# Kernel tuning notes

Hardware: AMD Instinct MI355X
Metric: run time of the kernel (lower is better)

Reference implementation:

```python
import jax, jax.numpy as jnp
import numpy as np

B, SQ, HID, NH, PAST = 8, 16, 1024, 16, 4096
DH = HID // NH
ROPE_BASE = 10000.0


def _rope(x, pos):
    # rotate-half RoPE applied over the full hidden dim (as in the module, rope
    # is built with hidden_size and applied before the head split)
    half = x.shape[-1] // 2
    inv_freq = 1.0 / (ROPE_BASE ** (jnp.arange(half, dtype=jnp.float32) / half))
    ang = pos[..., None].astype(jnp.float32) * inv_freq  # [B, S, half]
    cos, sin = jnp.cos(ang), jnp.sin(ang)
    x1, x2 = x[..., :half], x[..., half:]
    return jnp.concatenate([x1 * cos - x2 * sin, x2 * cos + x1 * sin], axis=-1).astype(x.dtype)


def setup_inputs() -> dict:
    key = jax.random.key(0)
    ks = jax.random.split(key, 16)
    s = 1.0 / np.sqrt(HID)
    return {
        "hidden_state": jax.random.normal(ks[0], (B, SQ, HID), jnp.float32),
        "attention_mask": jnp.zeros((B, SQ, SQ), jnp.float32),
        "past_key": jax.random.normal(ks[1], (B, NH, PAST, DH), jnp.float32),
        "past_value": jax.random.normal(ks[2], (B, NH, PAST, DH), jnp.float32),
        "position_ids": jax.random.randint(ks[3], (B, SQ), 0, 4200, jnp.int32),
        "Wq": jax.random.normal(ks[4], (HID, HID), jnp.float32) * s,
        "bq": jnp.zeros((HID,), jnp.float32),
        "Wk": jax.random.normal(ks[5], (HID, HID), jnp.float32) * s,
        "bk": jnp.zeros((HID,), jnp.float32),
        "Wv": jax.random.normal(ks[6], (HID, HID), jnp.float32) * s,
        "bv": jnp.zeros((HID,), jnp.float32),
        "Wo": jax.random.normal(ks[7], (HID, HID), jnp.float32) * s,
        "bo": jnp.zeros((HID,), jnp.float32),
    }


def reference(hidden_state, attention_mask, past_key, past_value, position_ids,
              Wq, bq, Wk, bk, Wv, bv, Wo, bo):
    b, sq, hid = hidden_state.shape
    nh = NH
    dh = hid // nh

    q = hidden_state @ Wq + bq
    k = hidden_state @ Wk + bk
    v = hidden_state @ Wv + bv

    q = _rope(q, position_ids)
    k = _rope(k, position_ids)

    # split heads -> [B, H, S, Dh]
    q = q.reshape(b, sq, nh, dh).transpose(0, 2, 1, 3)
    k = k.reshape(b, sq, nh, dh).transpose(0, 2, 1, 3)
    v = v.reshape(b, sq, nh, dh).transpose(0, 2, 1, 3)

    # KV-cache concat along the key/seq dim
    new_key = jnp.concatenate((past_key, k), axis=2)      # [B, H, Skv, Dh]
    new_value = jnp.concatenate((past_value, v), axis=2)
    skv_past = past_key.shape[2]
    mask = jnp.concatenate(
        (jnp.zeros((b, sq, skv_past), attention_mask.dtype), attention_mask), axis=2)

    scale = 1.0 / jnp.sqrt(jnp.asarray(dh, q.dtype))
    scores = jnp.einsum("bhqd,bhkd->bhqk", q, new_key) * scale + mask[:, None]
    probs = jax.nn.softmax(scores, axis=-1)
    ctx = jnp.einsum("bhqk,bhkd->bhqd", probs, new_value)  # [B, H, Sq, Dh]

    out = ctx.transpose(0, 2, 1, 3).reshape(b, sq, hid) @ Wo + bo
    return (out, new_key, new_value)
```

## Files before the change

kernel.cpp:

```cpp
#include <hip/hip_runtime.h>
#include <math.h>

#define BB   8
#define SQ   16
#define HIDD 1024
#define NHD  16
#define PAST 4096
#define DH   64
#define SKV  (PAST + SQ)
#define NTOK (BB * SQ)

__global__ __launch_bounds__(256) void gemm3(
    const float* __restrict__ A,
    const float* __restrict__ W0, const float* __restrict__ W1, const float* __restrict__ W2,
    const float* __restrict__ b0, const float* __restrict__ b1, const float* __restrict__ b2,
    float* __restrict__ O0, float* __restrict__ O1, float* __restrict__ O2)
{
    const int nt   = blockIdx.x;
    const int mt   = blockIdx.y;
    const int wsel = nt >> 4;
    const int col0 = (nt & 15) * 64;
    const int m0   = mt * 32;
    const float* W    = (wsel == 0) ? W0 : (wsel == 1) ? W1 : W2;
    const float* bias = (wsel == 0) ? b0 : (wsel == 1) ? b1 : b2;
    float*       Out  = (wsel == 0) ? O0 : (wsel == 1) ? O1 : O2;

    __shared__ float As[32][33];
    __shared__ float Bs[32][64];

    const int t    = threadIdx.x;
    const int tm   = t >> 4;
    const int tn   = t & 15;
    const int arow = t >> 3;
    const int acol = (t & 7) << 2;
    const int brow = t >> 4;
    const int bcol = (t & 15) << 2;

    float acc0[4] = {0.f,0.f,0.f,0.f};
    float acc1[4] = {0.f,0.f,0.f,0.f};

    for (int k0 = 0; k0 < HIDD; k0 += 32) {
        __syncthreads();
        float4 a4 = *(const float4*)(A + (size_t)(m0 + arow) * HIDD + k0 + acol);
        As[arow][acol+0] = a4.x; As[arow][acol+1] = a4.y;
        As[arow][acol+2] = a4.z; As[arow][acol+3] = a4.w;
        *(float4*)(&Bs[brow][bcol]) =
            *(const float4*)(W + (size_t)(k0 + brow) * HIDD + col0 + bcol);
        *(float4*)(&Bs[brow + 16][bcol]) =
            *(const float4*)(W + (size_t)(k0 + brow + 16) * HIDD + col0 + bcol);
        __syncthreads();
        #pragma unroll
        for (int kk = 0; kk < 32; ++kk) {
            const float  a0 = As[2*tm][kk];
            const float  a1 = As[2*tm + 1][kk];
            const float4 b4 = *(const float4*)(&Bs[kk][tn << 2]);
            acc0[0] += a0*b4.x; acc0[1] += a0*b4.y; acc0[2] += a0*b4.z; acc0[3] += a0*b4.w;
            acc1[0] += a1*b4.x; acc1[1] += a1*b4.y; acc1[2] += a1*b4.z; acc1[3] += a1*b4.w;
        }
    }
    const float4 bb = *(const float4*)(bias + col0 + (tn << 2));
    float* o0 = Out + (size_t)(m0 + 2*tm) * HIDD + col0 + (tn << 2);
    float* o1 = o0 + HIDD;
    o0[0] = acc0[0] + bb.x; o0[1] = acc0[1] + bb.y; o0[2] = acc0[2] + bb.z; o0[3] = acc0[3] + bb.w;
    o1[0] = acc1[0] + bb.x; o1[1] = acc1[1] + bb.y; o1[2] = acc1[2] + bb.z; o1[3] = acc1[3] + bb.w;
}

__global__ __launch_bounds__(256) void rope_scatter(
    const float* __restrict__ qr, const float* __restrict__ kr, const float* __restrict__ vr,
    const int* __restrict__ pos_ids,
    float* __restrict__ Qh, float* __restrict__ nk, float* __restrict__ nv)
{
    const int tok = blockIdx.x;
    const int b   = tok >> 4;
    const int s   = tok & 15;
    const float pos = (float)pos_ids[tok];
    const size_t rq = (size_t)tok * HIDD;
    for (int i = threadIdx.x; i < 512; i += 256) {
        const float inv = expf((float)i * (-9.210340371976184f / 512.0f));
        const float ang = pos * inv;
        const float c  = cosf(ang);
        const float sn = sinf(ang);
        const int h1 = i >> 6, d = i & 63;
        const int h2 = h1 + 8;
        float x1, x2;
        x1 = qr[rq + i]; x2 = qr[rq + i + 512];
        Qh[((size_t)(b*NHD + h1)*SQ + s)*DH + d] = x1*c - x2*sn;
        Qh[((size_t)(b*NHD + h2)*SQ + s)*DH + d] = x2*c + x1*sn;
        x1 = kr[rq + i]; x2 = kr[rq + i + 512];
        nk[((size_t)(b*NHD + h1)*SKV + PAST + s)*DH + d] = x1*c - x2*sn;
        nk[((size_t)(b*NHD + h2)*SKV + PAST + s)*DH + d] = x2*c + x1*sn;
        x1 = vr[rq + i]; x2 = vr[rq + i + 512];
        nv[((size_t)(b*NHD + h1)*SKV + PAST + s)*DH + d] = x1;
        nv[((size_t)(b*NHD + h2)*SKV + PAST + s)*DH + d] = x2;
    }
}

__global__ __launch_bounds__(256) void attn_partial(
    const float* __restrict__ pk, const float* __restrict__ pv,
    const float* __restrict__ Qh, const float* __restrict__ amask,
    float* __restrict__ nk, float* __restrict__ nv,
    float* __restrict__ pc, float* __restrict__ pm, float* __restrict__ pl)
{
    const int chunk = blockIdx.x;
    const int bh    = blockIdx.y;
    const int b     = bh >> 4;
    const int t     = threadIdx.x;
    const int w     = t >> 6;
    const int lane  = t & 63;
    const int qq    = lane >> 4;
    const int d4    = lane & 15;

    __shared__ float  Qs[SQ * DH];
    __shared__ float4 Ks[64 * 16];
    __shared__ float  Vs[64 * DH];
    __shared__ float4 Ps[4 * 64];

    {
        const int q = t >> 4, i = t & 15;
        float4 q4 = *(const float4*)(Qh + ((size_t)bh * SQ + q) * DH + 4*i);
        q4.x *= 0.125f; q4.y *= 0.125f; q4.z *= 0.125f; q4.w *= 0.125f;
        *(float4*)(&Qs[q * DH + 4*i]) = q4;
    }

    float m_r[4], l_r[4];
    #pragma unroll
    for (int q = 0; q < 4; ++q) { m_r[q] = -3.0e38f; l_r[q] = 0.0f; }
    float4 ctx = make_float4(0.f, 0.f, 0.f, 0.f);

    const int ntiles = (chunk == 7) ? 9 : 8;
    for (int tile = 0; tile < ntiles; ++tile) {
        __syncthreads();
        if (tile < 8) {
            const int k0 = chunk * 512 + tile * 64;
            #pragma unroll
            for (int p = 0; p < 4; ++p) {
                const int c = t + 256 * p;
                const int j = c >> 4, i = c & 15;
                const size_t po = ((size_t)bh * PAST + k0 + j) * DH + 4*i;
                const size_t no = ((size_t)bh * SKV  + k0 + j) * DH + 4*i;
                const float4 k4 = *(const float4*)(pk + po);
                *(float4*)(nk + no) = k4;
                Ks[j * 16 + (i ^ (j & 7))] = k4;
                const float4 v4 = *(const float4*)(pv + po);
                *(float4*)(nv + no) = v4;
                *(float4*)(&Vs[j * DH + 4*i]) = v4;
            }
        } else {
            const int j = t >> 4, i = t & 15;
            const size_t no = ((size_t)bh * SKV + PAST + j) * DH + 4*i;
            Ks[j * 16 + (i ^ (j & 7))] = *(const float4*)(nk + no);
            *(float4*)(&Vs[j * DH + 4*i]) = *(const float4*)(nv + no);
        }
        __syncthreads();

        const int jcount = (tile < 8) ? 64 : 16;

        float s[4];
        {
            float4 acc[4];
            #pragma unroll
            for (int q = 0; q < 4; ++q) acc[q] = make_float4(0.f,0.f,0.f,0.f);
            if (lane < jcount) {
                #pragma unroll
                for (int i = 0; i < 16; ++i) {
                    const float4 k4 = Ks[lane * 16 + (i ^ (lane & 7))];
                    #pragma unroll
                    for (int q = 0; q < 4; ++q) {
                        const float4 q4 = *(const float4*)(&Qs[(4*w + q) * DH + 4*i]);
                        acc[q].x += k4.x * q4.x; acc[q].y += k4.y * q4.y;
                        acc[q].z += k4.z * q4.z; acc[q].w += k4.w * q4.w;
                    }
                }
            }
            #pragma unroll
            for (int q = 0; q < 4; ++q)
                s[q] = (lane < jcount) ? (acc[q].x + acc[q].y + acc[q].z + acc[q].w)
                                       : -3.0e38f;
        }
        if (tile == 8 && lane < 16) {
            #pragma unroll
            for (int q = 0; q < 4; ++q)
                s[q] += amask[((size_t)b * SQ + 4*w + q) * SQ + lane];
        }

        float alpha[4], pjv[4];
        #pragma unroll
        for (int q = 0; q < 4; ++q) {
            float mx = s[q];
            #pragma unroll
            for (int off = 1; off < 64; off <<= 1)
                mx = fmaxf(mx, __shfl_xor(mx, off, 64));
            const float mnew = fmaxf(m_r[q], mx);
            alpha[q] = __expf(m_r[q] - mnew);
            const float p = __expf(s[q] - mnew);
            pjv[q] = p;
            float ps = p;
            #pragma unroll
            for (int off = 1; off < 64; off <<= 1)
                ps += __shfl_xor(ps, off, 64);
            l_r[q] = l_r[q] * alpha[q] + ps;
            m_r[q] = mnew;
        }
        {
            float4 pw;
            pw.x = pjv[0]; pw.y = pjv[1]; pw.z = pjv[2]; pw.w = pjv[3];
            Ps[w * 64 + lane] = pw;
        }

        const float asel = (qq == 0) ? alpha[0] : (qq == 1) ? alpha[1]
                         : (qq == 2) ? alpha[2] : alpha[3];
        ctx.x *= asel; ctx.y *= asel; ctx.z *= asel; ctx.w *= asel;

        const float* Pf = (const float*)&Ps[w * 64];
        for (int j = 0; j < jcount; ++j) {
            const float  p  = Pf[4*j + qq];
            const float4 v4 = *(const float4*)(&Vs[j * DH + 4*d4]);
            ctx.x += p * v4.x; ctx.y += p * v4.y; ctx.z += p * v4.z; ctx.w += p * v4.w;
        }
    }

    const int blk = bh * 8 + chunk;
    const int qg  = 4*w + qq;
    *(float4*)(pc + (size_t)blk * 1024 + qg * DH + 4*d4) = ctx;
    if (d4 == 0) {
        const float msel = (qq == 0) ? m_r[0] : (qq == 1) ? m_r[1] : (qq == 2) ? m_r[2] : m_r[3];
        const float lsel = (qq == 0) ? l_r[0] : (qq == 1) ? l_r[1] : (qq == 2) ? l_r[2] : l_r[3];
        pm[blk * 16 + qg] = msel;
        pl[blk * 16 + qg] = lsel;
    }
}

__global__ __launch_bounds__(256) void attn_reduce(
    const float* __restrict__ pc, const float* __restrict__ pm,
    const float* __restrict__ pl, float* __restrict__ ctxw)
{
    const int bh = blockIdx.x;
    const int b  = bh >> 4, h = bh & 15;
    const int t  = threadIdx.x;
    __shared__ float mg[SQ], li[SQ];
    if (t < SQ) {
        float m = -3.0e38f;
        #pragma unroll
        for (int c = 0; c < 8; ++c) m = fmaxf(m, pm[(bh*8 + c) * 16 + t]);
        float L = 0.f;
        #pragma unroll
        for (int c = 0; c < 8; ++c)
            L += pl[(bh*8 + c) * 16 + t] * __expf(pm[(bh*8 + c) * 16 + t] - m);
        mg[t] = m; li[t] = 1.0f / L;
    }
    __syncthreads();
    #pragma unroll
    for (int r = 0; r < 4; ++r) {
        const int idx = t + 256 * r;
        const int q = idx >> 6, d = idx & 63;
        float acc = 0.f;
        #pragma unroll
        for (int c = 0; c < 8; ++c)
            acc += pc[(size_t)(bh*8 + c) * 1024 + idx]
                 * __expf(pm[(bh*8 + c) * 16 + q] - mg[q]);
        ctxw[((size_t)(b*SQ + q) * NHD + h) * DH + d] = acc * li[q];
    }
}

extern "C" void kernel_launch(void* const* d_in, const int* in_sizes, int n_in,
                              void* d_out, int out_size, void* d_ws, size_t ws_size,
                              hipStream_t stream)
{
    const float* hidden = (const float*)d_in[0];
    const float* amask  = (const float*)d_in[1];
    const float* past_k = (const float*)d_in[2];
    const float* past_v = (const float*)d_in[3];
    const int*   pos    = (const int*)  d_in[4];
    const float* Wq = (const float*)d_in[5];  const float* bq = (const float*)d_in[6];
    const float* Wk = (const float*)d_in[7];  const float* bk = (const float*)d_in[8];
    const float* Wv = (const float*)d_in[9];  const float* bv = (const float*)d_in[10];
    const float* Wo = (const float*)d_in[11]; const float* bo = (const float*)d_in[12];

    float* out = (float*)d_out;
    float* nk  = out + (size_t)NTOK * HIDD;
    float* nv  = nk + (size_t)BB * NHD * SKV * DH;

    float* ws     = (float*)d_ws;
    float* q_raw  = ws;
    float* k_raw  = q_raw + 131072;
    float* v_raw  = k_raw + 131072;
    float* Qh     = v_raw + 131072;
    float* pc     = Qh    + 131072;
    float* pm     = pc    + 1024 * 1024;
    float* pl     = pm    + 1024 * 16;
    float* ctxw   = pl    + 1024 * 16;

    gemm3<<<dim3(48, 4), 256, 0, stream>>>(hidden, Wq, Wk, Wv, bq, bk, bv,
                                           q_raw, k_raw, v_raw);
    rope_scatter<<<NTOK, 256, 0, stream>>>(q_raw, k_raw, v_raw, pos, Qh, nk, nv);
    attn_partial<<<dim3(8, 128), 256, 0, stream>>>(past_k, past_v, Qh, amask,
                                                   nk, nv, pc, pm, pl);
    attn_reduce<<<128, 256, 0, stream>>>(pc, pm, pl, ctxw);
    gemm3<<<dim3(16, 4), 256, 0, stream>>>(ctxw, Wo, Wo, Wo, bo, bo, bo,
                                           out, out, out);
}
```

Before: 581.9 us.

## Split attention KV into more chunks and read V directly from global

```diff
diff --git a/kernel.cpp b/kernel.cpp
--- a/kernel.cpp
+++ b/kernel.cpp
@@ -76,10 +76,10 @@
     const float pos = (float)pos_ids[tok];
     const size_t rq = (size_t)tok * HIDD;
     for (int i = threadIdx.x; i < 512; i += 256) {
-        const float inv = expf((float)i * (-9.210340371976184f / 512.0f));
+        const float inv = __expf((float)i * (-9.210340371976184f / 512.0f));
         const float ang = pos * inv;
-        const float c  = cosf(ang);
-        const float sn = sinf(ang);
+        float c, sn;
+        __sincosf(ang, &sn, &c);
         const int h1 = i >> 6, d = i & 63;
         const int h2 = h1 + 8;
         float x1, x2;
@@ -95,11 +95,12 @@
     }
 }
 
-__global__ __launch_bounds__(256) void attn_partial(
+__global__ __launch_bounds__(256, 6) void attn_partial(
     const float* __restrict__ pk, const float* __restrict__ pv,
     const float* __restrict__ Qh, const float* __restrict__ amask,
     float* __restrict__ nk, float* __restrict__ nv,
-    float* __restrict__ pc, float* __restrict__ pm, float* __restrict__ pl)
+    float* __restrict__ pc, float* __restrict__ pm, float* __restrict__ pl,
+    const int nchunks)
 {
     const int chunk = blockIdx.x;
     const int bh    = blockIdx.y;
@@ -110,16 +111,22 @@
     const int qq    = lane >> 4;
     const int d4    = lane & 15;
 
+    const int kpc    = PAST / nchunks;
+    const int ktiles = kpc >> 6;
+
     __shared__ float  Qs[SQ * DH];
     __shared__ float4 Ks[64 * 16];
-    __shared__ float  Vs[64 * DH];
-    __shared__ float4 Ps[4 * 64];
+    __shared__ float  Ps2[4][4][64];
+
+    const int j0 = t >> 4;
+    const int i0 = t & 15;
+    const size_t pbase = (size_t)bh * PAST * DH;
+    const size_t nbase = (size_t)bh * SKV  * DH;
 
     {
-        const int q = t >> 4, i = t & 15;
-        float4 q4 = *(const float4*)(Qh + ((size_t)bh * SQ + q) * DH + 4*i);
+        float4 q4 = *(const float4*)(Qh + ((size_t)bh * SQ + j0) * DH + 4*i0);
         q4.x *= 0.125f; q4.y *= 0.125f; q4.z *= 0.125f; q4.w *= 0.125f;
-        *(float4*)(&Qs[q * DH + 4*i]) = q4;
+        *(float4*)(&Qs[j0 * DH + 4*i0]) = q4;
     }
 
     float m_r[4], l_r[4];
@@ -127,33 +134,29 @@
     for (int q = 0; q < 4; ++q) { m_r[q] = -3.0e38f; l_r[q] = 0.0f; }
     float4 ctx = make_float4(0.f, 0.f, 0.f, 0.f);
 
-    const int ntiles = (chunk == 7) ? 9 : 8;
+    const int ntiles = (chunk == nchunks - 1) ? (ktiles + 1) : ktiles;
     for (int tile = 0; tile < ntiles; ++tile) {
         __syncthreads();
-        if (tile < 8) {
-            const int k0 = chunk * 512 + tile * 64;
+        if (tile < ktiles) {
+            const int k0 = chunk * kpc + tile * 64;
             #pragma unroll
             for (int p = 0; p < 4; ++p) {
-                const int c = t + 256 * p;
-                const int j = c >> 4, i = c & 15;
-                const size_t po = ((size_t)bh * PAST + k0 + j) * DH + 4*i;
-                const size_t no = ((size_t)bh * SKV  + k0 + j) * DH + 4*i;
+                const int j = j0 + 16*p;
+                const size_t po = pbase + (size_t)(k0 + j) * DH + 4*i0;
+                const size_t no = nbase + (size_t)(k0 + j) * DH + 4*i0;
                 const float4 k4 = *(const float4*)(pk + po);
                 *(float4*)(nk + no) = k4;
-                Ks[j * 16 + (i ^ (j & 7))] = k4;
+                Ks[j * 16 + (i0 ^ (j & 7))] = k4;
                 const float4 v4 = *(const float4*)(pv + po);
                 *(float4*)(nv + no) = v4;
-                *(float4*)(&Vs[j * DH + 4*i]) = v4;
             }
         } else {
-            const int j = t >> 4, i = t & 15;
-            const size_t no = ((size_t)bh * SKV + PAST + j) * DH + 4*i;
-            Ks[j * 16 + (i ^ (j & 7))] = *(const float4*)(nk + no);
-            *(float4*)(&Vs[j * DH + 4*i]) = *(const float4*)(nv + no);
+            Ks[j0 * 16 + (i0 ^ (j0 & 7))] =
+                *(const float4*)(nk + nbase + (size_t)(PAST + j0) * DH + 4*i0);
         }
         __syncthreads();
 
-        const int jcount = (tile < 8) ? 64 : 16;
+        const int jcount = (tile < ktiles) ? 64 : 16;
 
         float s[4];
         {
@@ -177,7 +180,7 @@
                 s[q] = (lane < jcount) ? (acc[q].x + acc[q].y + acc[q].z + acc[q].w)
                                        : -3.0e38f;
         }
-        if (tile == 8 && lane < 16) {
+        if (tile == ktiles && lane < 16) {
             #pragma unroll
             for (int q = 0; q < 4; ++q)
                 s[q] += amask[((size_t)b * SQ + 4*w + q) * SQ + lane];
@@ -201,25 +204,34 @@
             l_r[q] = l_r[q] * alpha[q] + ps;
             m_r[q] = mnew;
         }
-        {
-            float4 pw;
-            pw.x = pjv[0]; pw.y = pjv[1]; pw.z = pjv[2]; pw.w = pjv[3];
-            Ps[w * 64 + lane] = pw;
-        }
+        #pragma unroll
+        for (int q = 0; q < 4; ++q)
+            Ps2[w][q][lane] = pjv[q];
 
         const float asel = (qq == 0) ? alpha[0] : (qq == 1) ? alpha[1]
                          : (qq == 2) ? alpha[2] : alpha[3];
         ctx.x *= asel; ctx.y *= asel; ctx.z *= asel; ctx.w *= asel;
 
-        const float* Pf = (const float*)&Ps[w * 64];
-        for (int j = 0; j < jcount; ++j) {
-            const float  p  = Pf[4*j + qq];
-            const float4 v4 = *(const float4*)(&Vs[j * DH + 4*d4]);
-            ctx.x += p * v4.x; ctx.y += p * v4.y; ctx.z += p * v4.z; ctx.w += p * v4.w;
-        }
-    }
-
-    const int blk = bh * 8 + chunk;
+        const float* Pq = &Ps2[w][0][0] + qq * 64;
+        const float* Vg = (tile < ktiles)
+                        ? (pv + pbase + (size_t)(chunk * kpc + tile * 64) * DH)
+                        : (nv + nbase + (size_t)PAST * DH);
+        const int j4 = jcount >> 2;
+        #pragma unroll 4
+        for (int jj = 0; jj < j4; ++jj) {
+            const float4 p4 = *(const float4*)(Pq + 4*jj);
+            const float4 v0 = *(const float4*)(Vg + (size_t)(4*jj + 0) * DH + 4*d4);
+            const float4 v1 = *(const float4*)(Vg + (size_t)(4*jj + 1) * DH + 4*d4);
+            const float4 v2 = *(const float4*)(Vg + (size_t)(4*jj + 2) * DH + 4*d4);
+            const float4 v3 = *(const float4*)(Vg + (size_t)(4*jj + 3) * DH + 4*d4);
+            ctx.x += p4.x*v0.x; ctx.y += p4.x*v0.y; ctx.z += p4.x*v0.z; ctx.w += p4.x*v0.w;
+            ctx.x += p4.y*v1.x; ctx.y += p4.y*v1.y; ctx.z += p4.y*v1.z; ctx.w += p4.y*v1.w;
+            ctx.x += p4.z*v2.x; ctx.y += p4.z*v2.y; ctx.z += p4.z*v2.z; ctx.w += p4.z*v2.w;
+            ctx.x += p4.w*v3.x; ctx.y += p4.w*v3.y; ctx.z += p4.w*v3.z; ctx.w += p4.w*v3.w;
+        }
+    }
+
+    const int blk = bh * nchunks + chunk;
     const int qg  = 4*w + qq;
     *(float4*)(pc + (size_t)blk * 1024 + qg * DH + 4*d4) = ctx;
     if (d4 == 0) {
@@ -232,21 +244,25 @@
 
 __global__ __launch_bounds__(256) void attn_reduce(
     const float* __restrict__ pc, const float* __restrict__ pm,
-    const float* __restrict__ pl, float* __restrict__ ctxw)
+    const float* __restrict__ pl, float* __restrict__ ctxw,
+    const int nchunks)
 {
     const int bh = blockIdx.x;
     const int b  = bh >> 4, h = bh & 15;
     const int t  = threadIdx.x;
-    __shared__ float mg[SQ], li[SQ];
+    __shared__ float wgt[16][SQ];
+    __shared__ float li[SQ];
     if (t < SQ) {
         float m = -3.0e38f;
-        #pragma unroll
-        for (int c = 0; c < 8; ++c) m = fmaxf(m, pm[(bh*8 + c) * 16 + t]);
+        for (int c = 0; c < nchunks; ++c)
+            m = fmaxf(m, pm[(bh*nchunks + c) * 16 + t]);
         float L = 0.f;
-        #pragma unroll
-        for (int c = 0; c < 8; ++c)
-            L += pl[(bh*8 + c) * 16 + t] * __expf(pm[(bh*8 + c) * 16 + t] - m);
-        mg[t] = m; li[t] = 1.0f / L;
+        for (int c = 0; c < nchunks; ++c) {
+            const float e = __expf(pm[(bh*nchunks + c) * 16 + t] - m);
+            L += pl[(bh*nchunks + c) * 16 + t] * e;
+            wgt[c][t] = e;
+        }
+        li[t] = 1.0f / L;
     }
     __syncthreads();
     #pragma unroll
@@ -254,10 +270,8 @@
         const int idx = t + 256 * r;
         const int q = idx >> 6, d = idx & 63;
         float acc = 0.f;
-        #pragma unroll
-        for (int c = 0; c < 8; ++c)
-            acc += pc[(size_t)(bh*8 + c) * 1024 + idx]
-                 * __expf(pm[(bh*8 + c) * 16 + q] - mg[q]);
+        for (int c = 0; c < nchunks; ++c)
+            acc += pc[(size_t)(bh*nchunks + c) * 1024 + idx] * wgt[c][q];
         ctxw[((size_t)(b*SQ + q) * NHD + h) * DH + d] = acc * li[q];
     }
 }
@@ -280,22 +294,31 @@
     float* nk  = out + (size_t)NTOK * HIDD;
     float* nv  = nk + (size_t)BB * NHD * SKV * DH;
 
+    auto ws_need = [](int nc) -> size_t {
+        return (size_t)(4 * 131072
+                        + nc * 128 * 1024
+                        + 2 * nc * 128 * 16
+                        + 131072)
+               * sizeof(float);
+    };
+    const int nchunks = (ws_size >= ws_need(16)) ? 16 : 8;
+
     float* ws     = (float*)d_ws;
     float* q_raw  = ws;
     float* k_raw  = q_raw + 131072;
     float* v_raw  = k_raw + 131072;
     float* Qh     = v_raw + 131072;
     float* pc     = Qh    + 131072;
-    float* pm     = pc    + 1024 * 1024;
-    float* pl     = pm    + 1024 * 16;
-    float* ctxw   = pl    + 1024 * 16;
+    float* pm     = pc    + (size_t)nchunks * 128 * 1024;
+    float* pl     = pm    + (size_t)nchunks * 128 * 16;
+    float* ctxw   = pl    + (size_t)nchunks * 128 * 16;
 
     gemm3<<<dim3(48, 4), 256, 0, stream>>>(hidden, Wq, Wk, Wv, bq, bk, bv,
                                            q_raw, k_raw, v_raw);
     rope_scatter<<<NTOK, 256, 0, stream>>>(q_raw, k_raw, v_raw, pos, Qh, nk, nv);
-    attn_partial<<<dim3(8, 128), 256, 0, stream>>>(past_k, past_v, Qh, amask,
-                                                   nk, nv, pc, pm, pl);
-    attn_reduce<<<128, 256, 0, stream>>>(pc, pm, pl, ctxw);
+    attn_partial<<<dim3(nchunks, 128), 256, 0, stream>>>(past_k, past_v, Qh, amask,
+                                                         nk, nv, pc, pm, pl, nchunks);
+    attn_reduce<<<128, 256, 0, stream>>>(pc, pm, pl, ctxw, nchunks);
     gemm3<<<dim3(16, 4), 256, 0, stream>>>(ctxw, Wo, Wo, Wo, bo, bo, bo,
                                            out, out, out);
 }
```

New measurement: 752.3 us. 1.29x slower.
